# Kernel optimization log

Measured on AMD Instinct MI355X. Metric: run time of the kernel, lower is better.

Reference implementation:

```python
import jax, jax.numpy as jnp
import numpy as np

# scaled DeepSeek-V2-style config
B, S, D, H, L = 1, 2048, 1024, 16, 2
E, K, I, SI, V = 8, 2, 512, 1024, 32000
Dh = D // H
IGNORE_IDX = -100


def setup_inputs() -> dict:
    key = jax.random.key(0)
    ks = jax.random.split(key, 18)
    f = lambda k, sh: jax.random.normal(k, sh, jnp.float32) * 0.02
    return {
        "src_tokens": jax.random.randint(ks[0], (B, S), 0, V, jnp.int32),
        "target": jax.random.randint(ks[1], (B, S), 0, V, jnp.int32),
        "embed": f(ks[2], (V, D)),
        "Wq": f(ks[3], (L, D, D)),
        "Wk": f(ks[4], (L, D, D)),
        "Wv": f(ks[5], (L, D, D)),
        "Wo": f(ks[6], (L, D, D)),
        "ln1": jnp.ones((L, D), jnp.float32),
        "ln2": jnp.ones((L, D), jnp.float32),
        "gate_w": f(ks[7], (L, E, D)),
        "gate_projs": f(ks[8], (L, E, I, D)),
        "up_projs": f(ks[9], (L, E, I, D)),
        "down_projs": f(ks[10], (L, E, D, I)),
        "sg": f(ks[11], (L, SI, D)),
        "su": f(ks[12], (L, SI, D)),
        "sd": f(ks[13], (L, D, SI)),
        "final_ln": jnp.ones((D,), jnp.float32),
        "lm_head": f(ks[14], (V, D)),
    }


def _rms(x, w, eps=1e-6):
    return x * jax.lax.rsqrt(jnp.mean(x * x, axis=-1, keepdims=True) + eps) * w


def _rot_half(x):
    x1, x2 = jnp.split(x, 2, axis=-1)
    return jnp.concatenate([-x2, x1], axis=-1)


def reference(src_tokens, target, embed, Wq, Wk, Wv, Wo, ln1, ln2, gate_w,
              gate_projs, up_projs, down_projs, sg, su, sd, final_ln, lm_head):
    # rotary tables [1,S,1,Dh]
    inv_freq = 1.0 / (10000.0 ** (jnp.arange(0, Dh, 2, dtype=jnp.float32) / Dh))
    ang = jnp.arange(S, dtype=jnp.float32)[:, None] * inv_freq[None, :]
    emb = jnp.concatenate([ang, ang], axis=-1)
    cos = jnp.cos(emb)[None, :, None, :]
    sin = jnp.sin(emb)[None, :, None, :]
    causal = jnp.tril(jnp.ones((S, S), bool))
    scale = 1.0 / float(np.sqrt(Dh))

    h = embed[src_tokens]  # [B,S,D]
    for l in range(L):
        x = _rms(h, ln1[l])
        q = (x @ Wq[l].T).reshape(B, S, H, Dh)
        k = (x @ Wk[l].T).reshape(B, S, H, Dh)
        v = (x @ Wv[l].T).reshape(B, S, H, Dh)
        q = q * cos + _rot_half(q) * sin
        k = k * cos + _rot_half(k) * sin
        sc = jnp.einsum('bqhd,bkhd->bhqk', q, k) * scale
        sc = jnp.where(causal, sc, -1e9)
        a = jax.nn.softmax(sc, axis=-1)
        o = jnp.einsum('bhqk,bkhd->bqhd', a, v).reshape(B, S, D)
        h = h + o @ Wo[l].T
        # DeepSeek-V2 MoE: softmax gate -> top-k combine over stacked experts
        x = _rms(h, ln2[l])
        probs = jax.nn.softmax(x @ gate_w[l].T, axis=-1)  # [B,S,E]
        topv, topi = jax.lax.top_k(probs, K)
        comb = (jax.nn.one_hot(topi, E, dtype=x.dtype) * topv[..., None]).sum(axis=2)  # [B,S,E]
        g = jnp.einsum('bsd,eid->bsei', x, gate_projs[l])
        u = jnp.einsum('bsd,eid->bsei', x, up_projs[l])
        act = jax.nn.silu(g) * u * comb[..., None]  # [B,S,E,I]
        routed = jnp.einsum('bsei,edi->bsd', act, down_projs[l])
        shared = (jax.nn.silu(x @ sg[l].T) * (x @ su[l].T)) @ sd[l].T
        h = h + routed + shared

    x = _rms(h, final_ln)
    logits = (x @ lm_head.T).reshape(-1, V).astype(jnp.float32)
    labels = target.reshape(-1)
    logp = jax.nn.log_softmax(logits, axis=-1)
    valid = labels != IGNORE_IDX
    safe = jnp.where(valid, labels, 0)
    nll = -jnp.take_along_axis(logp, safe[:, None], axis=1)[:, 0]
    loss = jnp.sum(jnp.where(valid, nll, 0.0))
    return loss
```

## Files before the change

kernel.cpp:

```cpp
#include <hip/hip_runtime.h>
#include <hip/hip_bf16.h>

#define S 2048
#define D 1024
#define H 16
#define DH 64
#define LAYERS 2
#define E 8
#define I_DIM 512
#define SI 1024
#define V 32000
#define NSTRIP 125

typedef unsigned short ushort_t;
typedef __attribute__((ext_vector_type(8))) short short8;
typedef __attribute__((ext_vector_type(4))) float floatx4;

__device__ __forceinline__ float bf2f(ushort_t u) {
  union { unsigned i; float f; } x;
  x.i = ((unsigned)u) << 16;
  return x.f;
}
__device__ __forceinline__ ushort_t f2bf(float f) {
  union { float f; unsigned u; } x; x.f = f;
  unsigned r = x.u + 0x7FFFu + ((x.u >> 16) & 1u);
  return (ushort_t)(r >> 16);
}
__device__ __forceinline__ int pack2(float a, float b) {
  return (int)((unsigned)f2bf(a) | ((unsigned)f2bf(b) << 16));
}

__device__ __forceinline__ int xcd_swz(int bid, int nwg) {
  int q = nwg >> 3, r = nwg & 7;
  int x = bid & 7, o = bid >> 3;
  return (x < r ? x * (q + 1) : r * (q + 1) + (x - r) * q) + o;
}

__device__ __forceinline__ void gl_lds16(const ushort_t* g, ushort_t* l) {
  __builtin_amdgcn_global_load_lds((const __attribute__((address_space(1))) void*)g,
                                   (__attribute__((address_space(3))) void*)l, 16, 0, 0);
}

__global__ __launch_bounds__(256) void convert_k(const float* __restrict__ in,
                                                 ushort_t* __restrict__ out, int n8) {
  int i = blockIdx.x * 256 + threadIdx.x;
  if (i >= n8) return;
  const float4* p = (const float4*)in + (size_t)i * 2;
  float4 a = p[0], b = p[1];
  int4 pk = {pack2(a.x, a.y), pack2(a.z, a.w), pack2(b.x, b.y), pack2(b.z, b.w)};
  ((int4*)out)[i] = pk;
}

__global__ __launch_bounds__(256) void embed_k(const int* __restrict__ tok,
                                               const float* __restrict__ emb,
                                               float* __restrict__ h) {
  int idx = blockIdx.x * 256 + threadIdx.x;
  if (idx >= S * D / 4) return;
  int s = idx >> 8;
  int d4 = idx & 255;
  int t = tok[s];
  float4 u = *(const float4*)(emb + (size_t)t * D + d4 * 4);
  *(float4*)(h + (size_t)s * D + d4 * 4) = u;
}

__global__ __launch_bounds__(256) void rmsnorm_k(const float* __restrict__ h,
                                                 const float* __restrict__ w,
                                                 ushort_t* __restrict__ xb) {
  int s = blockIdx.x, tid = threadIdx.x;
  __shared__ float red[256];
  float4 hv = *(const float4*)(h + (size_t)s * D + tid * 4);
  red[tid] = hv.x * hv.x + hv.y * hv.y + hv.z * hv.z + hv.w * hv.w;
  __syncthreads();
  for (int st = 128; st > 0; st >>= 1) {
    if (tid < st) red[tid] += red[tid + st];
    __syncthreads();
  }
  float inv = rsqrtf(red[0] * (1.0f / 1024.0f) + 1e-6f);
  float4 wv = *(const float4*)(w + tid * 4);
  int2 pk;
  pk.x = pack2(hv.x * inv * wv.x, hv.y * inv * wv.y);
  pk.y = pack2(hv.z * inv * wv.z, hv.w * inv * wv.w);
  *(int2*)(xb + (size_t)s * D + tid * 4) = pk;
}

template <int TM, int TN, int MODE, int EXPERT>
__global__ __launch_bounds__(256) void gbt_k(const ushort_t* __restrict__ A, int lda,
                                             const ushort_t* __restrict__ B, int ldb,
                                             void* __restrict__ Cv, int ldc, int K) {
  constexpr int WM = TM / 2, WN = TN / 2;
  constexpr int MT = WM / 16, NT = WN / 16;
  constexpr int CA = TM / 16, CB = TN / 16;
  __shared__ __align__(16) ushort_t As[TM * 32];
  __shared__ __align__(16) ushort_t Bs[TN * 32];
  int tid = threadIdx.x;
  int nwg = gridDim.x * gridDim.y;
  int sw = xcd_swz(blockIdx.x + gridDim.x * blockIdx.y, nwg);
  int bx = sw / gridDim.y, by = sw % gridDim.y;
  int n0 = bx * TN, m0 = by * TM;
  int w = tid >> 6, lane = tid & 63, quad = lane >> 4, l16 = lane & 15;
  int wm = (w >> 1) * WM, wn = (w & 1) * WN;
  int srow = lane >> 2, sko = (lane & 3) * 8;

  floatx4 acc[MT][NT];
#pragma unroll
  for (int mi = 0; mi < MT; mi++)
#pragma unroll
    for (int ni = 0; ni < NT; ni++)
      acc[mi][ni] = (floatx4){0.f, 0.f, 0.f, 0.f};

  for (int k0 = 0; k0 < K; k0 += 32) {
#pragma unroll
    for (int c = 0; c < CA; c += 4) {
      int ch = c + w;
      const ushort_t* gp = A + (size_t)(m0 + ch * 16 + srow) * lda + k0 + sko;
      gl_lds16(gp, As + ch * 512);
    }
#pragma unroll
    for (int c = 0; c < CB; c += 4) {
      int ch = c + w;
      const ushort_t* gp;
      if (EXPERT) {
        int kk = k0 + sko;
        int e = kk >> 9;
        gp = B + ((size_t)(e * D + n0 + ch * 16 + srow)) * I_DIM + (kk & 511);
      } else {
        gp = B + (size_t)(n0 + ch * 16 + srow) * ldb + k0 + sko;
      }
      gl_lds16(gp, Bs + ch * 512);
    }
    __syncthreads();
    short8 af[MT], bfv[NT];
#pragma unroll
    for (int mi = 0; mi < MT; mi++)
      af[mi] = *(const short8*)(As + (wm + mi * 16 + l16) * 32 + quad * 8);
#pragma unroll
    for (int ni = 0; ni < NT; ni++)
      bfv[ni] = *(const short8*)(Bs + (wn + ni * 16 + l16) * 32 + quad * 8);
#pragma unroll
    for (int mi = 0; mi < MT; mi++)
#pragma unroll
      for (int ni = 0; ni < NT; ni++)
        acc[mi][ni] = __builtin_amdgcn_mfma_f32_16x16x32_bf16(af[mi], bfv[ni],
                                                              acc[mi][ni], 0, 0, 0);
    __syncthreads();
  }
#pragma unroll
  for (int mi = 0; mi < MT; mi++) {
#pragma unroll
    for (int ni = 0; ni < NT; ni++) {
      int row_base = m0 + wm + mi * 16 + quad * 4;
      int col = n0 + wn + ni * 16 + l16;
#pragma unroll
      for (int r = 0; r < 4; r++) {
        if (MODE == 1) {
          ((ushort_t*)Cv)[(size_t)(row_base + r) * ldc + col] = f2bf(acc[mi][ni][r]);
        } else {
          float* cp = (float*)Cv + (size_t)(row_base + r) * ldc + col;
          float val = acc[mi][ni][r];
          if (MODE == 2) val += *cp;
          *cp = val;
        }
      }
    }
  }
}

#define GBODY(T, VMSTR, DOSTAGE)                                              \
  {                                                                           \
    if (DOSTAGE) STAGE((T) + 3);                                              \
    asm volatile("s_waitcnt vmcnt(" VMSTR ")" ::: "memory");                  \
    __builtin_amdgcn_sched_barrier(0);                                        \
    __builtin_amdgcn_s_barrier();                                             \
    __builtin_amdgcn_sched_barrier(0);                                        \
    asm volatile("" ::: "memory");                                            \
    const ushort_t* bA = smem + ((T) & 3) * 16384;                            \
    const ushort_t* bB = bA + 8192;                                           \
    short8 af[8], bfv[4];                                                     \
    _Pragma("unroll") for (int mi = 0; mi < 8; mi++) {                        \
      int row = wm + mi * 16 + l16;                                           \
      af[mi] = *(const short8*)(bA + row * 32 + ((quad ^ ((row >> 1) & 3)) << 3)); \
    }                                                                         \
    _Pragma("unroll") for (int ni = 0; ni < 4; ni++) {                        \
      int row = wn + ni * 16 + l16;                                           \
      bfv[ni] = *(const short8*)(bB + row * 32 + ((quad ^ ((row >> 1) & 3)) << 3)); \
    }                                                                         \
    __builtin_amdgcn_s_setprio(1);                                            \
    _Pragma("unroll") for (int mi = 0; mi < 8; mi++)                          \
      _Pragma("unroll") for (int ni = 0; ni < 4; ni++)                        \
        acc[mi][ni] = __builtin_amdgcn_mfma_f32_16x16x32_bf16(                \
            af[mi], bfv[ni], acc[mi][ni], 0, 0, 0);                           \
    __builtin_amdgcn_s_setprio(0);                                            \
    __builtin_amdgcn_sched_barrier(0);                                        \
    __builtin_amdgcn_s_barrier();                                             \
    asm volatile("" ::: "memory");                                            \
  }

template <int MODE>
__global__ __launch_bounds__(512, 2) void gemm256_k(
    const ushort_t* __restrict__ A, int lda,
    const ushort_t* __restrict__ B, int ldb,
    void* __restrict__ Cv, int ldc, int K,
    const int* __restrict__ target, float2* __restrict__ partial,
    float* __restrict__ tgt_l, int strip_base) {
  __shared__ __align__(16) ushort_t smem[4 * 16384];
  int tid = threadIdx.x;
  int wv = tid >> 6, lane = tid & 63, quad = lane >> 4, l16 = lane & 15;
  int wm = (wv >> 2) * 128, wn = (wv & 3) * 64;
  int nwg = gridDim.x * gridDim.y;
  int sw = xcd_swz(blockIdx.x + gridDim.x * blockIdx.y, nwg);
  int bx = sw / gridDim.y, by = sw % gridDim.y;
  int m0 = by * 256, n0 = bx * 256;
  int NT = K / 32;

  floatx4 acc[8][4];
#pragma unroll
  for (int mi = 0; mi < 8; mi++)
#pragma unroll
    for (int ni = 0; ni < 4; ni++) acc[mi][ni] = (floatx4){0.f, 0.f, 0.f, 0.f};

  auto STAGE = [&](int t) {
    int b = t & 3, k0 = t * 32;
    ushort_t* ba = smem + b * 16384;
#pragma unroll
    for (int ra = 0; ra < 2; ra++) {
      int Pb = ra * 8192 + tid * 16;
      int row = Pb >> 6;
      int kq = ((Pb >> 4) & 3) ^ ((row >> 1) & 3);
      gl_lds16(A + (size_t)(m0 + row) * lda + k0 + kq * 8,
               ba + ((ra * 8192 + wv * 1024) >> 1));
    }
#pragma unroll
    for (int rb = 0; rb < 2; rb++) {
      int Pb = rb * 8192 + tid * 16;
      int row = Pb >> 6;
      int kq = ((Pb >> 4) & 3) ^ ((row >> 1) & 3);
      gl_lds16(B + (size_t)(n0 + row) * ldb + k0 + kq * 8,
               ba + 8192 + ((rb * 8192 + wv * 1024) >> 1));
    }
  };

  STAGE(0);
  STAGE(1);
  STAGE(2);

  for (int t = 0; t < NT - 3; t++) GBODY(t, "12", 1);
  GBODY(NT - 3, "8", 0);
  GBODY(NT - 2, "4", 0);
  GBODY(NT - 1, "0", 0);

  if constexpr (MODE == 0) {
    ushort_t* C = (ushort_t*)Cv;
#pragma unroll
    for (int mi = 0; mi < 8; mi++)
#pragma unroll
      for (int ni = 0; ni < 4; ni++) {
        int rb = m0 + wm + mi * 16 + quad * 4;
        int col = n0 + wn + ni * 16 + l16;
#pragma unroll
        for (int r = 0; r < 4; r++)
          C[(size_t)(rb + r) * ldc + col] = f2bf(acc[mi][ni][r]);
      }
  } else {
    int strip = strip_base + bx;
    int n0g = strip * 256;
    float* pm = (float*)smem;
    float* pl = pm + 1024;
    int* tg = (int*)(pl + 1024);
    if (tid < 256) tg[tid] = target[m0 + tid];
    __syncthreads();
#pragma unroll
    for (int mi = 0; mi < 8; mi++) {
      float rmax[4], rsum[4];
#pragma unroll
      for (int r = 0; r < 4; r++) {
        float m = acc[mi][0][r];
#pragma unroll
        for (int ni = 1; ni < 4; ni++) m = fmaxf(m, acc[mi][ni][r]);
        rmax[r] = m;
      }
#pragma unroll
      for (int msk = 1; msk <= 8; msk <<= 1)
#pragma unroll
        for (int r = 0; r < 4; r++)
          rmax[r] = fmaxf(rmax[r], __shfl_xor(rmax[r], msk));
#pragma unroll
      for (int r = 0; r < 4; r++) {
        float ssum = 0.f;
#pragma unroll
        for (int ni = 0; ni < 4; ni++) ssum += __expf(acc[mi][ni][r] - rmax[r]);
        rsum[r] = ssum;
      }
#pragma unroll
      for (int msk = 1; msk <= 8; msk <<= 1)
#pragma unroll
        for (int r = 0; r < 4; r++) rsum[r] += __shfl_xor(rsum[r], msk);
      int rib = wm + mi * 16 + quad * 4;
#pragma unroll
      for (int r = 0; r < 4; r++) {
        int tt = tg[rib + r];
#pragma unroll
        for (int ni = 0; ni < 4; ni++) {
          int colg = n0g + wn + ni * 16 + l16;
          if (tt == colg) tgt_l[m0 + rib + r] = acc[mi][ni][r];
        }
      }
      if (l16 == 0) {
#pragma unroll
        for (int r = 0; r < 4; r++) {
          pm[(rib + r) * 4 + (wv & 3)] = rmax[r];
          pl[(rib + r) * 4 + (wv & 3)] = rsum[r];
        }
      }
    }
    __syncthreads();
    if (tid < 256) {
      float m = pm[tid * 4];
#pragma unroll
      for (int j = 1; j < 4; j++) m = fmaxf(m, pm[tid * 4 + j]);
      float l = 0.f;
#pragma unroll
      for (int j = 0; j < 4; j++) l += pl[tid * 4 + j] * __expf(pm[tid * 4 + j] - m);
      partial[(size_t)(m0 + tid) * NSTRIP + strip] = make_float2(m, l);
    }
  }
}

__global__ __launch_bounds__(256) void reduce_lse_k(const float2* __restrict__ partial,
                                                    const int* __restrict__ target,
                                                    const float* __restrict__ tgt_l,
                                                    float* __restrict__ nll) {
  int row = blockIdx.x * 256 + threadIdx.x;
  if (row >= S) return;
  float m = -1e30f, l = 0.f;
  for (int j = 0; j < NSTRIP; j++) {
    float2 pp = partial[(size_t)row * NSTRIP + j];
    float nm = fmaxf(m, pp.x);
    l = l * __expf(m - nm) + pp.y * __expf(pp.x - nm);
    m = nm;
  }
  int t = target[row];
  nll[row] = (t != -100) ? (logf(l) + m - tgt_l[row]) : 0.f;
}

__global__ __launch_bounds__(256) void sum_nll_k(const float* __restrict__ nll,
                                                 float* __restrict__ out) {
  __shared__ float red[256];
  int tid = threadIdx.x;
  float acc = 0.f;
  for (int s = tid; s < S; s += 256) acc += nll[s];
  red[tid] = acc;
  __syncthreads();
  for (int st = 128; st > 0; st >>= 1) {
    if (tid < st) red[tid] += red[tid + st];
    __syncthreads();
  }
  if (tid == 0) out[0] = red[0];
}

__global__ __launch_bounds__(256) void rope_tab_k(float2* __restrict__ tab) {
  int idx = blockIdx.x * 256 + threadIdx.x;
  int s = idx >> 5, i = idx & 31;
  float invf = expf(-(float)i * (9.210340371976184f / 32.0f));
  float ang = (float)s * invf;
  tab[idx] = make_float2(cosf(ang), sinf(ang));
}

__global__ __launch_bounds__(256) void rope_k(ushort_t* __restrict__ qkv,
                                              const float2* __restrict__ tab) {
  int idx = blockIdx.x * 256 + threadIdx.x;
  int s = idx >> 9;
  int r = idx & 511;
  int hd = r >> 5, i = r & 31;
  float2 cs = tab[(s << 5) | i];
  float c = cs.x, sn = cs.y;
  size_t base = (size_t)s * 3072 + hd * DH + i;
  float q1 = bf2f(qkv[base]), q2 = bf2f(qkv[base + 32]);
  qkv[base] = f2bf(q1 * c - q2 * sn);
  qkv[base + 32] = f2bf(q2 * c + q1 * sn);
  float k1 = bf2f(qkv[base + 1024]), k2 = bf2f(qkv[base + 1024 + 32]);
  qkv[base + 1024] = f2bf(k1 * c - k2 * sn);
  qkv[base + 1024 + 32] = f2bf(k2 * c + k1 * sn);
}

#define PSTR 72
__global__ __launch_bounds__(256) void flash_attn_k(const ushort_t* __restrict__ q,
                                                    const ushort_t* __restrict__ k,
                                                    const ushort_t* __restrict__ v,
                                                    ushort_t* __restrict__ out) {
  __shared__ __align__(16) ushort_t QPs[64 * PSTR];
  __shared__ __align__(16) ushort_t Ks[64 * PSTR];
  __shared__ __align__(16) ushort_t Vt[64 * PSTR];
  int nwg = gridDim.x * gridDim.y;
  int sw = xcd_swz(blockIdx.x + gridDim.x * blockIdx.y, nwg);
  int hh = sw / gridDim.x;
  int qt = (gridDim.x - 1) - (sw % gridDim.x);
  int q0 = qt * 64;
  int tid = threadIdx.x;
  int w = tid >> 6, lane = tid & 63, quad = lane >> 4, l16 = lane & 15;

  {
    int row = tid >> 2, c0 = (tid & 3) * 16;
    const ushort_t* p = q + (size_t)(q0 + row) * 3072 + hh * DH + c0;
    *(int4*)(QPs + row * PSTR + c0) = ((const int4*)p)[0];
    *(int4*)(QPs + row * PSTR + c0 + 8) = ((const int4*)p)[1];
  }
  __syncthreads();
  short8 af[2];
  af[0] = *(const short8*)(QPs + (w * 16 + l16) * PSTR + quad * 8);
  af[1] = *(const short8*)(QPs + (w * 16 + l16) * PSTR + 32 + quad * 8);

  float m_i[4], l_i[4];
  floatx4 oacc[4];
#pragma unroll
  for (int r = 0; r < 4; r++) { m_i[r] = -1e30f; l_i[r] = 0.f; }
#pragma unroll
  for (int ni = 0; ni < 4; ni++) oacc[ni] = (floatx4){0.f, 0.f, 0.f, 0.f};

  for (int kt = 0; kt <= qt; kt++) {
    int kb = kt * 64;
    __syncthreads();
    {
      int row = tid >> 2, c0 = (tid & 3) * 16;
      const ushort_t* p = k + (size_t)(kb + row) * 3072 + hh * DH + c0;
      *(int4*)(Ks + row * PSTR + c0) = ((const int4*)p)[0];
      *(int4*)(Ks + row * PSTR + c0 + 8) = ((const int4*)p)[1];
    }
    {
      const ushort_t* p = v + (size_t)(kb + lane) * 3072 + hh * DH + w * 16;
      ushort_t tmp[16];
      *(int4*)tmp = ((const int4*)p)[0];
      *(int4*)(tmp + 8) = ((const int4*)p)[1];
#pragma unroll
      for (int j = 0; j < 16; j++)
        Vt[(w * 16 + j) * PSTR + lane] = tmp[j];
    }
    __syncthreads();
    floatx4 sfr[4];
#pragma unroll
    for (int ni = 0; ni < 4; ni++) sfr[ni] = (floatx4){0.f, 0.f, 0.f, 0.f};
#pragma unroll
    for (int ks = 0; ks < 2; ks++) {
#pragma unroll
      for (int ni = 0; ni < 4; ni++) {
        short8 bfr = *(const short8*)(Ks + (ni * 16 + l16) * PSTR + ks * 32 + quad * 8);
        sfr[ni] = __builtin_amdgcn_mfma_f32_16x16x32_bf16(af[ks], bfr, sfr[ni], 0, 0, 0);
      }
    }
    int qrow = q0 + w * 16 + quad * 4;
#pragma unroll
    for (int ni = 0; ni < 4; ni++) {
#pragma unroll
      for (int r = 0; r < 4; r++) {
        float s = sfr[ni][r] * 0.125f;
        if (kt == qt) {
          int key = kb + ni * 16 + l16;
          if (key > qrow + r) s = -1e30f;
        }
        sfr[ni][r] = s;
      }
    }
    float tmax[4];
#pragma unroll
    for (int r = 0; r < 4; r++)
      tmax[r] = fmaxf(fmaxf(sfr[0][r], sfr[1][r]), fmaxf(sfr[2][r], sfr[3][r]));
#pragma unroll
    for (int msk = 1; msk <= 8; msk <<= 1)
#pragma unroll
      for (int r = 0; r < 4; r++)
        tmax[r] = fmaxf(tmax[r], __shfl_xor(tmax[r], msk));
    float alpha[4];
#pragma unroll
    for (int r = 0; r < 4; r++) {
      float mn = fmaxf(m_i[r], tmax[r]);
      alpha[r] = __expf(m_i[r] - mn);
      m_i[r] = mn;
    }
    float tsum[4] = {0.f, 0.f, 0.f, 0.f};
#pragma unroll
    for (int ni = 0; ni < 4; ni++) {
#pragma unroll
      for (int r = 0; r < 4; r++) {
        float p = __expf(sfr[ni][r] - m_i[r]);
        sfr[ni][r] = p;
        tsum[r] += p;
      }
    }
#pragma unroll
    for (int msk = 1; msk <= 8; msk <<= 1)
#pragma unroll
      for (int r = 0; r < 4; r++)
        tsum[r] += __shfl_xor(tsum[r], msk);
#pragma unroll
    for (int r = 0; r < 4; r++) l_i[r] = l_i[r] * alpha[r] + tsum[r];
#pragma unroll
    for (int ni = 0; ni < 4; ni++)
#pragma unroll
      for (int r = 0; r < 4; r++) oacc[ni][r] *= alpha[r];
#pragma unroll
    for (int ni = 0; ni < 4; ni++)
#pragma unroll
      for (int r = 0; r < 4; r++)
        QPs[(w * 16 + quad * 4 + r) * PSTR + ni * 16 + l16] = f2bf(sfr[ni][r]);
    __threadfence_block();
#pragma unroll
    for (int ks = 0; ks < 2; ks++) {
      short8 pf = *(const short8*)(QPs + (w * 16 + l16) * PSTR + ks * 32 + quad * 8);
#pragma unroll
      for (int ni = 0; ni < 4; ni++) {
        short8 bfr = *(const short8*)(Vt + (ni * 16 + l16) * PSTR + ks * 32 + quad * 8);
        oacc[ni] = __builtin_amdgcn_mfma_f32_16x16x32_bf16(pf, bfr, oacc[ni], 0, 0, 0);
      }
    }
  }
#pragma unroll
  for (int r = 0; r < 4; r++) l_i[r] = 1.0f / l_i[r];
#pragma unroll
  for (int ni = 0; ni < 4; ni++) {
#pragma unroll
    for (int r = 0; r < 4; r++) {
      int row = q0 + w * 16 + quad * 4 + r;
      out[(size_t)row * D + hh * DH + ni * 16 + l16] = f2bf(oacc[ni][r] * l_i[r]);
    }
  }
}

__global__ __launch_bounds__(256) void gate_top2_k(const ushort_t* __restrict__ x,
                                                   const float* __restrict__ gw,
                                                   float* __restrict__ comb) {
  int s = blockIdx.x, tid = threadIdx.x;
  __shared__ float xs[D];
  __shared__ float red[E][32];
  __shared__ float lg[E];
  for (int i = tid; i < D; i += 256) xs[i] = bf2f(x[(size_t)s * D + i]);
  __syncthreads();
  int e = tid >> 5, j = tid & 31;
  float p = 0.f;
  for (int d = j; d < D; d += 32) p += xs[d] * gw[e * D + d];
  red[e][j] = p;
  __syncthreads();
  if (tid < E) {
    float sum = 0.f;
    for (int jj = 0; jj < 32; jj++) sum += red[tid][jj];
    lg[tid] = sum;
  }
  __syncthreads();
  if (tid == 0) {
    float m = lg[0];
    for (int i = 1; i < E; i++) m = fmaxf(m, lg[i]);
    float pr[E];
    float ssum = 0.f;
    for (int i = 0; i < E; i++) { pr[i] = __expf(lg[i] - m); ssum += pr[i]; }
    float rs = 1.0f / ssum;
    for (int i = 0; i < E; i++) pr[i] *= rs;
    int b1 = 0;
    for (int i = 1; i < E; i++) if (pr[i] > pr[b1]) b1 = i;
    int b2 = -1;
    for (int i = 0; i < E; i++) {
      if (i == b1) continue;
      if (b2 < 0 || pr[i] > pr[b2]) b2 = i;
    }
    for (int i = 0; i < E; i++)
      comb[(size_t)s * E + i] = (i == b1) ? pr[b1] : ((i == b2) ? pr[b2] : 0.f);
  }
}

__global__ __launch_bounds__(256) void silu_moe_k(const ushort_t* __restrict__ gu,
                                                  const float* __restrict__ comb,
                                                  ushort_t* __restrict__ act) {
  int idx = blockIdx.x * 256 + threadIdx.x;
  int s = idx >> 12, rem = idx & 4095;
  int e = rem >> 9;
  size_t gi = (size_t)s * 8192 + rem;
  float gv = bf2f(gu[gi]);
  float sig = 1.0f / (1.0f + __expf(-gv));
  act[idx] = f2bf(gv * sig * bf2f(gu[gi + 4096]) * comb[(size_t)s * E + e]);
}

__global__ __launch_bounds__(256) void silu2_k(ushort_t* __restrict__ xgu) {
  int idx = blockIdx.x * 256 + threadIdx.x;
  int s = idx >> 10, i = idx & 1023;
  size_t a = (size_t)s * 2048 + i;
  float av = bf2f(xgu[a]);
  float sig = 1.0f / (1.0f + __expf(-av));
  xgu[a] = f2bf(av * sig * bf2f(xgu[a + 1024]));
}

extern "C" void kernel_launch(void* const* d_in, const int* in_sizes, int n_in,
                              void* d_out, int out_size, void* d_ws, size_t ws_size,
                              hipStream_t stream) {
  const int* src_tokens   = (const int*)d_in[0];
  const int* target       = (const int*)d_in[1];
  const float* embed      = (const float*)d_in[2];
  const float* Wq         = (const float*)d_in[3];
  const float* Wk         = (const float*)d_in[4];
  const float* Wv         = (const float*)d_in[5];
  const float* Wo         = (const float*)d_in[6];
  const float* ln1        = (const float*)d_in[7];
  const float* ln2        = (const float*)d_in[8];
  const float* gate_w     = (const float*)d_in[9];
  const float* gate_projs = (const float*)d_in[10];
  const float* up_projs   = (const float*)d_in[11];
  const float* down_projs = (const float*)d_in[12];
  const float* sg         = (const float*)d_in[13];
  const float* su         = (const float*)d_in[14];
  const float* sd         = (const float*)d_in[15];
  const float* final_ln   = (const float*)d_in[16];
  const float* lm_head    = (const float*)d_in[17];
  float* out = (float*)d_out;

  const size_t SD = (size_t)S * D;
  char* p = (char*)d_ws;
  float* h        = (float*)p;    p += SD * 4;
  ushort_t* qkvb  = (ushort_t*)p; p += (size_t)S * 3072 * 2;
  ushort_t* xb    = (ushort_t*)p; p += SD * 2;
  ushort_t* aob   = (ushort_t*)p; p += SD * 2;
  ushort_t* gu    = (ushort_t*)p; p += (size_t)S * 8192 * 2;
  ushort_t* act_bf= (ushort_t*)p; p += (size_t)S * 4096 * 2;
  ushort_t* xgu   = (ushort_t*)p; p += (size_t)S * 2048 * 2;
  float* comb     = (float*)p;    p += (size_t)S * E * 4;
  float* tgt_l    = (float*)p;    p += S * 4;
  float* nll      = (float*)p;    p += S * 4;
  float2* partial = (float2*)p;   p += (size_t)S * NSTRIP * 8;
  float2* rtab    = (float2*)p;   p += (size_t)S * 32 * 8;
  ushort_t* qkv_w = (ushort_t*)p; p += (size_t)LAYERS * 3072 * D * 2;
  ushort_t* Wo_bf = (ushort_t*)p; p += (size_t)LAYERS * D * D * 2;
  ushort_t* gu_w  = (ushort_t*)p; p += (size_t)LAYERS * 8192 * D * 2;
  ushort_t* dp_bf = (ushort_t*)p; p += (size_t)LAYERS * E * D * I_DIM * 2;
  ushort_t* sgsu_w= (ushort_t*)p; p += (size_t)LAYERS * 2048 * D * 2;
  ushort_t* sd_bf = (ushort_t*)p; p += (size_t)LAYERS * D * SI * 2;
  ushort_t* lmc   = gu;

  auto conv = [&](const float* src, ushort_t* dst, size_t n) {
    convert_k<<<(int)(n / 8 / 256), 256, 0, stream>>>(src, dst, (int)(n / 8));
  };
  const size_t DD = (size_t)D * D;
  for (int l = 0; l < LAYERS; l++) {
    conv(Wq + l * DD, qkv_w + (size_t)l * 3072 * D, DD);
    conv(Wk + l * DD, qkv_w + (size_t)l * 3072 * D + 1024 * D, DD);
    conv(Wv + l * DD, qkv_w + (size_t)l * 3072 * D + 2048 * D, DD);
    conv(gate_projs + (size_t)l * 4096 * D, gu_w + (size_t)l * 8192 * D, 4096 * (size_t)D);
    conv(up_projs + (size_t)l * 4096 * D, gu_w + (size_t)l * 8192 * D + 4096 * D, 4096 * (size_t)D);
    conv(sg + l * (size_t)SI * D, sgsu_w + (size_t)l * 2048 * D, (size_t)SI * D);
    conv(su + l * (size_t)SI * D, sgsu_w + (size_t)l * 2048 * D + 1024 * D, (size_t)SI * D);
  }
  conv(Wo, Wo_bf, LAYERS * DD);
  conv(down_projs, dp_bf, (size_t)LAYERS * E * D * I_DIM);
  conv(sd, sd_bf, (size_t)LAYERS * D * SI);

  rope_tab_k<<<(S * 32) / 256, 256, 0, stream>>>(rtab);
  embed_k<<<(S * D / 4) / 256, 256, 0, stream>>>(src_tokens, embed, h);

  for (int l = 0; l < LAYERS; l++) {
    rmsnorm_k<<<S, 256, 0, stream>>>(h, ln1 + (size_t)l * D, xb);
    gbt_k<128, 128, 1, 0><<<dim3(3072 / 128, S / 128), 256, 0, stream>>>(
        xb, D, qkv_w + (size_t)l * 3072 * D, D, qkvb, 3072, D);
    rope_k<<<(S * H * 32) / 256, 256, 0, stream>>>(qkvb, rtab);
    flash_attn_k<<<dim3(S / 64, H), 256, 0, stream>>>(qkvb, qkvb + 1024, qkvb + 2048, aob);
    gbt_k<64, 128, 2, 0><<<dim3(D / 128, S / 64), 256, 0, stream>>>(
        aob, D, Wo_bf + (size_t)l * DD, D, h, D, D);

    rmsnorm_k<<<S, 256, 0, stream>>>(h, ln2 + (size_t)l * D, xb);
    gate_top2_k<<<S, 256, 0, stream>>>(xb, gate_w + (size_t)l * E * D, comb);
    gemm256_k<0><<<dim3(8192 / 256, S / 256), 512, 0, stream>>>(
        xb, D, gu_w + (size_t)l * 8192 * D, D, gu, 8192, D,
        nullptr, nullptr, nullptr, 0);
    silu_moe_k<<<(S * 4096) / 256, 256, 0, stream>>>(gu, comb, act_bf);
    gbt_k<64, 128, 2, 1><<<dim3(D / 128, S / 64), 256, 0, stream>>>(
        act_bf, E * I_DIM, dp_bf + (size_t)l * E * D * I_DIM, 0, h, D, E * I_DIM);
    gbt_k<128, 128, 1, 0><<<dim3(2048 / 128, S / 128), 256, 0, stream>>>(
        xb, D, sgsu_w + (size_t)l * 2048 * D, D, xgu, 2048, D);
    silu2_k<<<(S * SI) / 256, 256, 0, stream>>>(xgu);
    gbt_k<64, 128, 2, 0><<<dim3(D / 128, S / 64), 256, 0, stream>>>(
        xgu, 2048, sd_bf + (size_t)l * D * SI, SI, h, D, SI);
  }

  rmsnorm_k<<<S, 256, 0, stream>>>(h, final_ln, xb);
  {
    conv(lm_head, lmc, (size_t)16384 * D);
    gemm256_k<1><<<dim3(64, S / 256), 512, 0, stream>>>(
        xb, D, lmc, D, nullptr, 0, D, target, partial, tgt_l, 0);
    conv(lm_head + (size_t)16384 * D, lmc, (size_t)15616 * D);
    gemm256_k<1><<<dim3(61, S / 256), 512, 0, stream>>>(
        xb, D, lmc, D, nullptr, 0, D, target, partial, tgt_l, 64);
  }
  reduce_lse_k<<<S / 256, 256, 0, stream>>>(partial, target, tgt_l, nll);
  sum_nll_k<<<1, 256, 0, stream>>>(nll, out);
}
```

Measured before the change: 1.285 ms.

## Fuse SiLU-gating epilogues into gate/up GEMMs via interleaved weight rows

Gate and up projection weights are now converted into a row-interleaved bf16 layout, so each gate column sits next to its matching up column in the GEMM output. The MoE and shared-expert GEMMs then apply silu(g)*u (times the routing weight for MoE) in their epilogue using a lane shuffle, and write half-width activations directly. This removes the separate silu_moe and silu2 passes and the full-width intermediate writes and reads. gemm256_k also gains an M-tile template parameter (128 for the MoE GEMM) and moves from a 4-stage to a 2-stage LDS pipeline, which frees shared memory but may expose more load latency.

Measured after the change: 1.248 ms. -2.8%, faster.

```diff
diff --git a/kernel.cpp b/kernel.cpp
--- a/kernel.cpp
+++ b/kernel.cpp
@@ -49,6 +49,19 @@
   float4 a = p[0], b = p[1];
   int4 pk = {pack2(a.x, a.y), pack2(a.z, a.w), pack2(b.x, b.y), pack2(b.z, b.w)};
   ((int4*)out)[i] = pk;
+}
+
+__global__ __launch_bounds__(256) void convert_ilv_k(const float* __restrict__ in,
+                                                     ushort_t* __restrict__ out,
+                                                     int n8, int off) {
+  int i = blockIdx.x * 256 + threadIdx.x;
+  if (i >= n8) return;
+  int row = i >> 7;
+  int c8 = i & 127;
+  const float4* p = (const float4*)in + (size_t)i * 2;
+  float4 a = p[0], b = p[1];
+  int4 pk = {pack2(a.x, a.y), pack2(a.z, a.w), pack2(b.x, b.y), pack2(b.z, b.w)};
+  ((int4*)(out + ((size_t)(2 * row + off)) * D))[c8] = pk;
 }
 
 __global__ __launch_bounds__(256) void embed_k(const int* __restrict__ tok,
@@ -154,6 +167,14 @@
       for (int r = 0; r < 4; r++) {
         if (MODE == 1) {
           ((ushort_t*)Cv)[(size_t)(row_base + r) * ldc + col] = f2bf(acc[mi][ni][r]);
+        } else if (MODE == 3) {
+          float g = acc[mi][ni][r];
+          float u = __shfl_xor(g, 1);
+          if (!(l16 & 1)) {
+            float sig = 1.0f / (1.0f + __expf(-g));
+            ((ushort_t*)Cv)[(size_t)(row_base + r) * ldc + (col >> 1)] =
+                f2bf(g * sig * u);
+          }
         } else {
           float* cp = (float*)Cv + (size_t)(row_base + r) * ldc + col;
           float val = acc[mi][ni][r];
@@ -167,16 +188,16 @@
 
 #define GBODY(T, VMSTR, DOSTAGE)                                              \
   {                                                                           \
-    if (DOSTAGE) STAGE((T) + 3);                                              \
+    if (DOSTAGE) STAGE((T) + 1);                                              \
     asm volatile("s_waitcnt vmcnt(" VMSTR ")" ::: "memory");                  \
     __builtin_amdgcn_sched_barrier(0);                                        \
     __builtin_amdgcn_s_barrier();                                             \
     __builtin_amdgcn_sched_barrier(0);                                        \
     asm volatile("" ::: "memory");                                            \
-    const ushort_t* bA = smem + ((T) & 3) * 16384;                            \
-    const ushort_t* bB = bA + 8192;                                           \
-    short8 af[8], bfv[4];                                                     \
-    _Pragma("unroll") for (int mi = 0; mi < 8; mi++) {                        \
+    const ushort_t* bA = smem + ((T) & 1) * SLOT;                             \
+    const ushort_t* bB = bA + TM2 * 32;                                       \
+    short8 af[MT], bfv[4];                                                    \
+    _Pragma("unroll") for (int mi = 0; mi < MT; mi++) {                       \
       int row = wm + mi * 16 + l16;                                           \
       af[mi] = *(const short8*)(bA + row * 32 + ((quad ^ ((row >> 1) & 3)) << 3)); \
     }                                                                         \
@@ -185,7 +206,7 @@
       bfv[ni] = *(const short8*)(bB + row * 32 + ((quad ^ ((row >> 1) & 3)) << 3)); \
     }                                                                         \
     __builtin_amdgcn_s_setprio(1);                                            \
-    _Pragma("unroll") for (int mi = 0; mi < 8; mi++)                          \
+    _Pragma("unroll") for (int mi = 0; mi < MT; mi++)                         \
       _Pragma("unroll") for (int ni = 0; ni < 4; ni++)                        \
         acc[mi][ni] = __builtin_amdgcn_mfma_f32_16x16x32_bf16(                \
             af[mi], bfv[ni], acc[mi][ni], 0, 0, 0);                           \
@@ -195,34 +216,37 @@
     asm volatile("" ::: "memory");                                            \
   }
 
-template <int MODE>
+template <int TM2, int MODE>
 __global__ __launch_bounds__(512, 2) void gemm256_k(
     const ushort_t* __restrict__ A, int lda,
     const ushort_t* __restrict__ B, int ldb,
     void* __restrict__ Cv, int ldc, int K,
     const int* __restrict__ target, float2* __restrict__ partial,
-    float* __restrict__ tgt_l, int strip_base) {
-  __shared__ __align__(16) ushort_t smem[4 * 16384];
+    float* __restrict__ tgt_l, const float* __restrict__ combp, int strip_base) {
+  constexpr int MT = TM2 / 32;
+  constexpr int SLOT = (TM2 + 256) * 32;
+  constexpr int RA = TM2 / 128;
+  __shared__ __align__(16) ushort_t smem[2 * SLOT];
   int tid = threadIdx.x;
   int wv = tid >> 6, lane = tid & 63, quad = lane >> 4, l16 = lane & 15;
-  int wm = (wv >> 2) * 128, wn = (wv & 3) * 64;
+  int wm = (wv >> 2) * (TM2 / 2), wn = (wv & 3) * 64;
   int nwg = gridDim.x * gridDim.y;
   int sw = xcd_swz(blockIdx.x + gridDim.x * blockIdx.y, nwg);
   int bx = sw / gridDim.y, by = sw % gridDim.y;
-  int m0 = by * 256, n0 = bx * 256;
+  int m0 = by * TM2, n0 = bx * 256;
   int NT = K / 32;
 
-  floatx4 acc[8][4];
-#pragma unroll
-  for (int mi = 0; mi < 8; mi++)
+  floatx4 acc[MT][4];
+#pragma unroll
+  for (int mi = 0; mi < MT; mi++)
 #pragma unroll
     for (int ni = 0; ni < 4; ni++) acc[mi][ni] = (floatx4){0.f, 0.f, 0.f, 0.f};
 
   auto STAGE = [&](int t) {
-    int b = t & 3, k0 = t * 32;
-    ushort_t* ba = smem + b * 16384;
-#pragma unroll
-    for (int ra = 0; ra < 2; ra++) {
+    int b = t & 1, k0 = t * 32;
+    ushort_t* ba = smem + b * SLOT;
+#pragma unroll
+    for (int ra = 0; ra < RA; ra++) {
       int Pb = ra * 8192 + tid * 16;
       int row = Pb >> 6;
       int kq = ((Pb >> 4) & 3) ^ ((row >> 1) & 3);
@@ -235,23 +259,23 @@
       int row = Pb >> 6;
       int kq = ((Pb >> 4) & 3) ^ ((row >> 1) & 3);
       gl_lds16(B + (size_t)(n0 + row) * ldb + k0 + kq * 8,
-               ba + 8192 + ((rb * 8192 + wv * 1024) >> 1));
+               ba + TM2 * 32 + ((rb * 8192 + wv * 1024) >> 1));
     }
   };
 
   STAGE(0);
-  STAGE(1);
-  STAGE(2);
-
-  for (int t = 0; t < NT - 3; t++) GBODY(t, "12", 1);
-  GBODY(NT - 3, "8", 0);
-  GBODY(NT - 2, "4", 0);
-  GBODY(NT - 1, "0", 0);
+  if constexpr (RA == 2) {
+    for (int t = 0; t < NT - 1; t++) GBODY(t, "4", 1);
+    GBODY(NT - 1, "0", 0);
+  } else {
+    for (int t = 0; t < NT - 1; t++) GBODY(t, "3", 1);
+    GBODY(NT - 1, "0", 0);
+  }
 
   if constexpr (MODE == 0) {
     ushort_t* C = (ushort_t*)Cv;
 #pragma unroll
-    for (int mi = 0; mi < 8; mi++)
+    for (int mi = 0; mi < MT; mi++)
 #pragma unroll
       for (int ni = 0; ni < 4; ni++) {
         int rb = m0 + wm + mi * 16 + quad * 4;
@@ -259,17 +283,40 @@
 #pragma unroll
         for (int r = 0; r < 4; r++)
           C[(size_t)(rb + r) * ldc + col] = f2bf(acc[mi][ni][r]);
+      }
+  } else if constexpr (MODE == 2) {
+    float* cb = (float*)smem;
+    int e = n0 >> 10;
+    if (tid < TM2) cb[tid] = combp[(size_t)(m0 + tid) * E + e];
+    __syncthreads();
+    ushort_t* Cp = (ushort_t*)Cv;
+#pragma unroll
+    for (int mi = 0; mi < MT; mi++)
+#pragma unroll
+      for (int ni = 0; ni < 4; ni++) {
+        int lrow = wm + mi * 16 + quad * 4;
+        int colg = n0 + wn + ni * 16 + l16;
+#pragma unroll
+        for (int r = 0; r < 4; r++) {
+          float g = acc[mi][ni][r];
+          float u = __shfl_xor(g, 1);
+          if (!(l16 & 1)) {
+            float sig = 1.0f / (1.0f + __expf(-g));
+            Cp[(size_t)(m0 + lrow + r) * 4096 + (colg >> 1)] =
+                f2bf(g * sig * u * cb[lrow + r]);
+          }
+        }
       }
   } else {
     int strip = strip_base + bx;
     int n0g = strip * 256;
     float* pm = (float*)smem;
-    float* pl = pm + 1024;
-    int* tg = (int*)(pl + 1024);
-    if (tid < 256) tg[tid] = target[m0 + tid];
-    __syncthreads();
-#pragma unroll
-    for (int mi = 0; mi < 8; mi++) {
+    float* pl = pm + TM2 * 4;
+    int* tg = (int*)(pl + TM2 * 4);
+    if (tid < TM2) tg[tid] = target[m0 + tid];
+    __syncthreads();
+#pragma unroll
+    for (int mi = 0; mi < MT; mi++) {
       float rmax[4], rsum[4];
 #pragma unroll
       for (int r = 0; r < 4; r++) {
@@ -313,7 +360,7 @@
       }
     }
     __syncthreads();
-    if (tid < 256) {
+    if (tid < TM2) {
       float m = pm[tid * 4];
 #pragma unroll
       for (int j = 1; j < 4; j++) m = fmaxf(m, pm[tid * 4 + j]);
@@ -562,27 +609,6 @@
     for (int i = 0; i < E; i++)
       comb[(size_t)s * E + i] = (i == b1) ? pr[b1] : ((i == b2) ? pr[b2] : 0.f);
   }
-}
-
-__global__ __launch_bounds__(256) void silu_moe_k(const ushort_t* __restrict__ gu,
-                                                  const float* __restrict__ comb,
-                                                  ushort_t* __restrict__ act) {
-  int idx = blockIdx.x * 256 + threadIdx.x;
-  int s = idx >> 12, rem = idx & 4095;
-  int e = rem >> 9;
-  size_t gi = (size_t)s * 8192 + rem;
-  float gv = bf2f(gu[gi]);
-  float sig = 1.0f / (1.0f + __expf(-gv));
-  act[idx] = f2bf(gv * sig * bf2f(gu[gi + 4096]) * comb[(size_t)s * E + e]);
-}
-
-__global__ __launch_bounds__(256) void silu2_k(ushort_t* __restrict__ xgu) {
-  int idx = blockIdx.x * 256 + threadIdx.x;
-  int s = idx >> 10, i = idx & 1023;
-  size_t a = (size_t)s * 2048 + i;
-  float av = bf2f(xgu[a]);
-  float sig = 1.0f / (1.0f + __expf(-av));
-  xgu[a] = f2bf(av * sig * bf2f(xgu[a + 1024]));
 }
 
 extern "C" void kernel_launch(void* const* d_in, const int* in_sizes, int n_in,
@@ -638,10 +664,14 @@
     conv(Wq + l * DD, qkv_w + (size_t)l * 3072 * D, DD);
     conv(Wk + l * DD, qkv_w + (size_t)l * 3072 * D + 1024 * D, DD);
     conv(Wv + l * DD, qkv_w + (size_t)l * 3072 * D + 2048 * D, DD);
-    conv(gate_projs + (size_t)l * 4096 * D, gu_w + (size_t)l * 8192 * D, 4096 * (size_t)D);
-    conv(up_projs + (size_t)l * 4096 * D, gu_w + (size_t)l * 8192 * D + 4096 * D, 4096 * (size_t)D);
-    conv(sg + l * (size_t)SI * D, sgsu_w + (size_t)l * 2048 * D, (size_t)SI * D);
-    conv(su + l * (size_t)SI * D, sgsu_w + (size_t)l * 2048 * D + 1024 * D, (size_t)SI * D);
+    convert_ilv_k<<<(4096 * D / 8) / 256, 256, 0, stream>>>(
+        gate_projs + (size_t)l * 4096 * D, gu_w + (size_t)l * 8192 * D, 4096 * D / 8, 0);
+    convert_ilv_k<<<(4096 * D / 8) / 256, 256, 0, stream>>>(
+        up_projs + (size_t)l * 4096 * D, gu_w + (size_t)l * 8192 * D, 4096 * D / 8, 1);
+    convert_ilv_k<<<(1024 * D / 8) / 256, 256, 0, stream>>>(
+        sg + (size_t)l * SI * D, sgsu_w + (size_t)l * 2048 * D, 1024 * D / 8, 0);
+    convert_ilv_k<<<(1024 * D / 8) / 256, 256, 0, stream>>>(
+        su + (size_t)l * SI * D, sgsu_w + (size_t)l * 2048 * D, 1024 * D / 8, 1);
   }
   conv(Wo, Wo_bf, LAYERS * DD);
   conv(down_projs, dp_bf, (size_t)LAYERS * E * D * I_DIM);
@@ -661,27 +691,25 @@
 
     rmsnorm_k<<<S, 256, 0, stream>>>(h, ln2 + (size_t)l * D, xb);
     gate_top2_k<<<S, 256, 0, stream>>>(xb, gate_w + (size_t)l * E * D, comb);
-    gemm256_k<0><<<dim3(8192 / 256, S / 256), 512, 0, stream>>>(
-        xb, D, gu_w + (size_t)l * 8192 * D, D, gu, 8192, D,
-        nullptr, nullptr, nullptr, 0);
-    silu_moe_k<<<(S * 4096) / 256, 256, 0, stream>>>(gu, comb, act_bf);
+    gemm256_k<128, 2><<<dim3(8192 / 256, S / 128), 512, 0, stream>>>(
+        xb, D, gu_w + (size_t)l * 8192 * D, D, act_bf, 4096, D,
+        nullptr, nullptr, nullptr, comb, 0);
     gbt_k<64, 128, 2, 1><<<dim3(D / 128, S / 64), 256, 0, stream>>>(
         act_bf, E * I_DIM, dp_bf + (size_t)l * E * D * I_DIM, 0, h, D, E * I_DIM);
-    gbt_k<128, 128, 1, 0><<<dim3(2048 / 128, S / 128), 256, 0, stream>>>(
-        xb, D, sgsu_w + (size_t)l * 2048 * D, D, xgu, 2048, D);
-    silu2_k<<<(S * SI) / 256, 256, 0, stream>>>(xgu);
+    gbt_k<128, 128, 3, 0><<<dim3(2048 / 128, S / 128), 256, 0, stream>>>(
+        xb, D, sgsu_w + (size_t)l * 2048 * D, D, xgu, 1024, D);
     gbt_k<64, 128, 2, 0><<<dim3(D / 128, S / 64), 256, 0, stream>>>(
-        xgu, 2048, sd_bf + (size_t)l * D * SI, SI, h, D, SI);
+        xgu, 1024, sd_bf + (size_t)l * D * SI, SI, h, D, SI);
   }
 
   rmsnorm_k<<<S, 256, 0, stream>>>(h, final_ln, xb);
   {
     conv(lm_head, lmc, (size_t)16384 * D);
-    gemm256_k<1><<<dim3(64, S / 256), 512, 0, stream>>>(
-        xb, D, lmc, D, nullptr, 0, D, target, partial, tgt_l, 0);
+    gemm256_k<256, 1><<<dim3(64, S / 256), 512, 0, stream>>>(
+        xb, D, lmc, D, nullptr, 0, D, target, partial, tgt_l, nullptr, 0);
     conv(lm_head + (size_t)16384 * D, lmc, (size_t)15616 * D);
-    gemm256_k<1><<<dim3(61, S / 256), 512, 0, stream>>>(
-        xb, D, lmc, D, nullptr, 0, D, target, partial, tgt_l, 64);
+    gemm256_k<256, 1><<<dim3(61, S / 256), 512, 0, stream>>>(
+        xb, D, lmc, D, nullptr, 0, D, target, partial, tgt_l, nullptr, 64);
   }
   reduce_lse_k<<<S / 256, 256, 0, stream>>>(partial, target, tgt_l, nll);
   sum_nll_k<<<1, 256, 0, stream>>>(nll, out);
```
